# Kernel optimization log

Measured on AMD Instinct MI355X. Metric: run time of the kernel, lower is better.

Reference implementation:

```python
import jax, jax.numpy as jnp
import numpy as np

N_NODES = 30000
N_EDGES = 480000
IN_CH = 256
OUT_CH = 64
HEADS = 4
NEG_SLOPE = 0.2


def setup_inputs() -> dict:
    key = jax.random.key(0)
    ks = jax.random.split(key, 12)
    glorot = lambda k, shape: jax.random.normal(k, shape, jnp.float32) * (2.0 / (shape[0] + shape[-1])) ** 0.5
    x = jax.random.normal(ks[0], (N_NODES, IN_CH), jnp.float32)
    edge_index = jax.random.randint(ks[1], (2, N_EDGES), 0, N_NODES, dtype=jnp.int64)
    # gat1: in -> heads*out, concat=True
    W1 = glorot(ks[2], (IN_CH, HEADS * OUT_CH))
    att_src1 = glorot(ks[3], (HEADS, OUT_CH)) * 0.1
    att_dst1 = glorot(ks[4], (HEADS, OUT_CH)) * 0.1
    b1 = jnp.zeros((HEADS * OUT_CH,), jnp.float32)
    # gat2: heads*out -> out, 1 head
    W2 = glorot(ks[5], (HEADS * OUT_CH, OUT_CH))
    att_src2 = glorot(ks[6], (1, OUT_CH)) * 0.1
    att_dst2 = glorot(ks[7], (1, OUT_CH)) * 0.1
    b2 = jnp.zeros((OUT_CH,), jnp.float32)
    return {"x": x, "edge_index": edge_index, "W1": W1, "att_src1": att_src1,
            "att_dst1": att_dst1, "b1": b1, "W2": W2, "att_src2": att_src2,
            "att_dst2": att_dst2, "b2": b2}


def gat_conv(x, src, dst, W, att_src, att_dst, bias, heads, out_ch):
    """PyG GATConv (eval mode, add_self_loops already applied to src/dst).
    x: [N, F_in]; src/dst: [E] int; W: [F_in, heads*out_ch]; att_*: [heads, out_ch].
    Returns [N, heads*out_ch] (concatenated heads)."""
    N = x.shape[0]
    h = (x @ W).reshape(N, heads, out_ch)                     # [N,H,C]
    a_src = jnp.einsum('nhc,hc->nh', h, att_src)              # [N,H]
    a_dst = jnp.einsum('nhc,hc->nh', h, att_dst)              # [N,H]
    alpha = jax.nn.leaky_relu(a_src[src] + a_dst[dst], NEG_SLOPE)  # [E,H]
    # numerically stable softmax over edges grouped by destination node
    m = jax.ops.segment_max(alpha, dst, num_segments=N)       # [N,H]
    e = jnp.exp(alpha - m[dst])                               # [E,H]
    denom = jax.ops.segment_sum(e, dst, num_segments=N)       # [N,H]
    coef = e / denom[dst]                                     # [E,H]
    msg = h[src] * coef[:, :, None]                           # [E,H,C]
    out = jax.ops.segment_sum(msg, dst, num_segments=N)       # [N,H,C]
    return out.reshape(N, heads * out_ch) + bias


def reference(x, edge_index, W1, att_src1, att_dst1, b1, W2, att_src2, att_dst2, b2):
    N = x.shape[0]
    loops = jnp.arange(N, dtype=edge_index.dtype)
    src = jnp.concatenate([edge_index[0], loops])
    dst = jnp.concatenate([edge_index[1], loops])
    h = gat_conv(x, src, dst, W1, att_src1, att_dst1, b1, HEADS, OUT_CH)
    h = jax.nn.elu(h)
    out = gat_conv(h, src, dst, W2, att_src2, att_dst2, b2, 1, OUT_CH)
    return out
```

## Files before the change

kernel.cpp:

```cpp
#include <hip/hip_runtime.h>
#include <hip/hip_bf16.h>
#include <math.h>


#define NN 30000
#define NE 480000
#define CAP 64
#define GB1 469
#define FB1 469

typedef __attribute__((ext_vector_type(8))) short bf16x8;
typedef __attribute__((ext_vector_type(4))) float f32x4;

static constexpr size_t au(size_t x) { return (x + 255) & ~(size_t)255; }

static constexpr size_t SZ_H1B = (size_t)NN * 256 * 2;
static constexpr size_t SZ_HB  = (size_t)NN * 256 * 2;
static constexpr size_t SZ_H2B = (size_t)NN * 64 * 2;
static constexpr size_t SZ_W1T = 256 * 256 * 2;
static constexpr size_t SZ_W2T = 64 * 256 * 2;
static constexpr size_t SZ_AS1 = (size_t)NN * 4 * 4;
static constexpr size_t SZ_AS2 = (size_t)NN * 4;
static constexpr size_t SZ_CNT = (size_t)NN * 4;
static constexpr size_t SZ_CSR = (size_t)NN * CAP * 4;

static constexpr size_t OFF_H1B = 0;
static constexpr size_t OFF_HB  = OFF_H1B + au(SZ_H1B);
static constexpr size_t OFF_H2B = OFF_HB  + au(SZ_HB);
static constexpr size_t OFF_W1T = OFF_H2B + au(SZ_H2B);
static constexpr size_t OFF_W2T = OFF_W1T + au(SZ_W1T);
static constexpr size_t OFF_AS1 = OFF_W2T + au(SZ_W2T);
static constexpr size_t OFF_AD1 = OFF_AS1 + au(SZ_AS1);
static constexpr size_t OFF_AS2 = OFF_AD1 + au(SZ_AS1);
static constexpr size_t OFF_AD2 = OFF_AS2 + au(SZ_AS2);
static constexpr size_t OFF_CNT = OFF_AD2 + au(SZ_AS2);
static constexpr size_t OFF_CSR = OFF_CNT + au(SZ_CNT);

__device__ __forceinline__ float lrelu(float x) { return x > 0.f ? x : 0.2f * x; }
__device__ __forceinline__ float elu1(float x)  { return x > 0.f ? x : expm1f(x); }

__device__ __forceinline__ float bf2f(ushort u) {
    union { unsigned i; float f; } v; v.i = ((unsigned)u) << 16; return v.f;
}
__device__ __forceinline__ ushort f2bf(float f) {
    union { float f; unsigned i; } v; v.f = f;
    unsigned x = v.i;
    return (ushort)((x + 0x7FFFu + ((x >> 16) & 1u)) >> 16);
}


__global__ __launch_bounds__(256) void prep_kernel(const float* __restrict__ W1,
                                                   const float* __restrict__ W2,
                                                   ushort* __restrict__ w1t,
                                                   ushort* __restrict__ w2t,
                                                   int* __restrict__ cnt) {
    int i = blockIdx.x * 256 + threadIdx.x;
    if (i < NN) cnt[i] = 0;
    if (i < 256 * 256) {
        int r = i >> 8, c = i & 255;
        w1t[c * 256 + r] = f2bf(W1[i]);
    } else {
        int j = i - 256 * 256;
        if (j < 256 * 64) {
            int r = j >> 6, c = j & 63;
            w2t[c * 256 + r] = f2bf(W2[j]);
        }
    }
}


__global__ __launch_bounds__(256)
void g1f_kernel(const float* __restrict__ X, const ushort* __restrict__ BT,
                const float* __restrict__ att_s, const float* __restrict__ att_d,
                ushort* __restrict__ C, float* __restrict__ a_s,
                float* __restrict__ a_d, int M,
                const int* __restrict__ esrc, const int* __restrict__ edst,
                int* __restrict__ cnt, int* __restrict__ csr, int ne) {
    if (blockIdx.x & 1) {
        const int T = FB1 * 256;
        const int t = (blockIdx.x >> 1) * 256 + threadIdx.x;
        int s[4], d[4], pos[4];
        bool v[4];
#pragma unroll
        for (int j = 0; j < 4; ++j) {
            int i = t + j * T;
            v[j] = (i < ne);
            if (v[j]) { s[j] = esrc[i]; d[j] = edst[i]; }
        }
#pragma unroll
        for (int j = 0; j < 4; ++j)
            if (v[j]) pos[j] = atomicAdd(&cnt[d[j]], 1);
#pragma unroll
        for (int j = 0; j < 4; ++j)
            if (v[j] && pos[j] < CAP) csr[d[j] * CAP + pos[j]] = s[j];
        return;
    }
    constexpr int K = 256, N = 256;
    __shared__ float s_s[64 * 4], s_d[64 * 4];
    const int lane = threadIdx.x & 63;
    const int wn   = threadIdx.x >> 6;
    const int r  = lane & 15;
    const int kq = lane >> 4;
    const long rbase = (long)(blockIdx.x >> 1) * 64;
    const int  col0  = wn * 64;

    f32x4 acc[4][4] = {};
#pragma unroll 2
    for (int ks = 0; ks < K / 32; ++ks) {
        const int kb = ks * 32 + kq * 8;
        bf16x8 bfr[4];
#pragma unroll
        for (int n = 0; n < 4; ++n)
            bfr[n] = *(const bf16x8*)(BT + (long)(col0 + n * 16 + r) * K + kb);
#pragma unroll
        for (int m = 0; m < 4; ++m) {
            long rr = rbase + m * 16 + r; if (rr >= M) rr = M - 1;
            const float* xp = X + rr * (long)K + kb;
            f32x4 x0 = *(const f32x4*)xp;
            f32x4 x1 = *(const f32x4*)(xp + 4);
            bf16x8 afr;
            afr[0] = (short)f2bf(x0[0]); afr[1] = (short)f2bf(x0[1]);
            afr[2] = (short)f2bf(x0[2]); afr[3] = (short)f2bf(x0[3]);
            afr[4] = (short)f2bf(x1[0]); afr[5] = (short)f2bf(x1[1]);
            afr[6] = (short)f2bf(x1[2]); afr[7] = (short)f2bf(x1[3]);
#pragma unroll
            for (int n = 0; n < 4; ++n)
                acc[m][n] = __builtin_amdgcn_mfma_f32_16x16x32_bf16(afr, bfr[n], acc[m][n], 0, 0, 0);
        }
    }
#pragma unroll
    for (int m = 0; m < 4; ++m)
#pragma unroll
        for (int reg = 0; reg < 4; ++reg) {
            long rr = rbase + m * 16 + kq * 4 + reg;
            if (rr < M) {
                ushort* cp = C + rr * (long)N + col0 + r;
#pragma unroll
                for (int n = 0; n < 4; ++n) cp[n * 16] = f2bf(acc[m][n][reg]);
            }
        }
    float aws[4], awd[4];
#pragma unroll
    for (int n = 0; n < 4; ++n) {
        aws[n] = att_s[col0 + n * 16 + r];
        awd[n] = att_d[col0 + n * 16 + r];
    }
#pragma unroll
    for (int m = 0; m < 4; ++m)
#pragma unroll
        for (int reg = 0; reg < 4; ++reg) {
            float ps = acc[m][0][reg] * aws[0] + acc[m][1][reg] * aws[1]
                     + acc[m][2][reg] * aws[2] + acc[m][3][reg] * aws[3];
            float pd = acc[m][0][reg] * awd[0] + acc[m][1][reg] * awd[1]
                     + acc[m][2][reg] * awd[2] + acc[m][3][reg] * awd[3];
#pragma unroll
            for (int off = 1; off < 16; off <<= 1) {
                ps += __shfl_xor(ps, off, 64);
                pd += __shfl_xor(pd, off, 64);
            }
            if (r == 0) {
                int rl = m * 16 + kq * 4 + reg;
                s_s[rl * 4 + wn] = ps;
                s_d[rl * 4 + wn] = pd;
            }
        }
    __syncthreads();
    int t = threadIdx.x;
    long row = rbase + (t >> 2);
    if (row < M) {
        a_s[row * 4 + (t & 3)] = s_s[t];
        a_d[row * 4 + (t & 3)] = s_d[t];
    }
}


__global__ __launch_bounds__(256)
void gemm_att2_kernel(const ushort* __restrict__ A, const ushort* __restrict__ BT,
                      const float* __restrict__ att_s, const float* __restrict__ att_d,
                      ushort* __restrict__ C, float* __restrict__ a_s,
                      float* __restrict__ a_d, int M) {
    constexpr int K = 256, N = 64;
    const int lane = threadIdx.x & 63;
    const int wm   = threadIdx.x >> 6;
    const int r  = lane & 15;
    const int kq = lane >> 4;
    const long rbase = (long)blockIdx.x * 64 + wm * 16;

    f32x4 acc[4] = {};
#pragma unroll
    for (int ks = 0; ks < K / 32; ++ks) {
        const int kb = ks * 32 + kq * 8;
        long rr = rbase + r; if (rr >= M) rr = M - 1;
        bf16x8 afr = *(const bf16x8*)(A + rr * (long)K + kb);
#pragma unroll
        for (int n = 0; n < 4; ++n) {
            bf16x8 bfr = *(const bf16x8*)(BT + (long)(n * 16 + r) * K + kb);
            acc[n] = __builtin_amdgcn_mfma_f32_16x16x32_bf16(afr, bfr, acc[n], 0, 0, 0);
        }
    }
#pragma unroll
    for (int reg = 0; reg < 4; ++reg) {
        long rr = rbase + kq * 4 + reg;
        if (rr < M) {
            ushort* cp = C + rr * (long)N + r;
#pragma unroll
            for (int n = 0; n < 4; ++n) cp[n * 16] = f2bf(acc[n][reg]);
        }
    }
    float aws[4], awd[4];
#pragma unroll
    for (int n = 0; n < 4; ++n) {
        aws[n] = att_s[n * 16 + r];
        awd[n] = att_d[n * 16 + r];
    }
#pragma unroll
    for (int reg = 0; reg < 4; ++reg) {
        float ps = acc[0][reg] * aws[0] + acc[1][reg] * aws[1]
                 + acc[2][reg] * aws[2] + acc[3][reg] * aws[3];
        float pd = acc[0][reg] * awd[0] + acc[1][reg] * awd[1]
                 + acc[2][reg] * awd[2] + acc[3][reg] * awd[3];
#pragma unroll
        for (int off = 1; off < 16; off <<= 1) {
            ps += __shfl_xor(ps, off, 64);
            pd += __shfl_xor(pd, off, 64);
        }
        if (r == 0) {
            long row = rbase + kq * 4 + reg;
            if (row < M) { a_s[row] = ps; a_d[row] = pd; }
        }
    }
}


__global__ __launch_bounds__(256) void agg1_kernel(const ushort* __restrict__ h1b,
                                                   const float* __restrict__ a_s,
                                                   const float* __restrict__ a_d,
                                                   const int* __restrict__ cnt,
                                                   const int* __restrict__ csr,
                                                   const float* __restrict__ b1,
                                                   ushort* __restrict__ hb, int n_nodes) {
    const int lane = threadIdx.x & 63;
    const int n = blockIdx.x * 4 + (threadIdx.x >> 6);
    if (n >= n_nodes) return;
    const int head = lane >> 4;
    const float ad = a_d[(size_t)n * 4 + head];
    float acc0, acc1, acc2, acc3, ws;
    {
        float w = __expf(lrelu(a_s[(size_t)n * 4 + head] + ad));
        ushort4 hv = *(const ushort4*)(h1b + (size_t)n * 256 + 4 * lane);
        acc0 = w * bf2f(hv.x); acc1 = w * bf2f(hv.y);
        acc2 = w * bf2f(hv.z); acc3 = w * bf2f(hv.w);
        ws = w;
    }
    const int* bucket = csr + (size_t)n * CAP;
    const int deg = min(cnt[n], CAP);
    int e = 0;
    for (; e + 8 <= deg; e += 8) {
        int s[8];
#pragma unroll
        for (int j = 0; j < 8; ++j) s[j] = bucket[e + j];
        float q[8];
        ushort4 hv[8];
#pragma unroll
        for (int j = 0; j < 8; ++j) {
            q[j] = a_s[(size_t)s[j] * 4 + head];
            hv[j] = *(const ushort4*)(h1b + (size_t)s[j] * 256 + 4 * lane);
        }
#pragma unroll
        for (int j = 0; j < 8; ++j) {
            float w = __expf(lrelu(q[j] + ad));
            acc0 = fmaf(w, bf2f(hv[j].x), acc0);
            acc1 = fmaf(w, bf2f(hv[j].y), acc1);
            acc2 = fmaf(w, bf2f(hv[j].z), acc2);
            acc3 = fmaf(w, bf2f(hv[j].w), acc3);
            ws += w;
        }
    }
    for (; e + 4 <= deg; e += 4) {
        int s[4];
#pragma unroll
        for (int j = 0; j < 4; ++j) s[j] = bucket[e + j];
        float q[4];
        ushort4 hv[4];
#pragma unroll
        for (int j = 0; j < 4; ++j) {
            q[j] = a_s[(size_t)s[j] * 4 + head];
            hv[j] = *(const ushort4*)(h1b + (size_t)s[j] * 256 + 4 * lane);
        }
#pragma unroll
        for (int j = 0; j < 4; ++j) {
            float w = __expf(lrelu(q[j] + ad));
            acc0 = fmaf(w, bf2f(hv[j].x), acc0);
            acc1 = fmaf(w, bf2f(hv[j].y), acc1);
            acc2 = fmaf(w, bf2f(hv[j].z), acc2);
            acc3 = fmaf(w, bf2f(hv[j].w), acc3);
            ws += w;
        }
    }
    for (; e < deg; ++e) {
        int s = bucket[e];
        float w = __expf(lrelu(a_s[(size_t)s * 4 + head] + ad));
        ushort4 hv = *(const ushort4*)(h1b + (size_t)s * 256 + 4 * lane);
        acc0 = fmaf(w, bf2f(hv.x), acc0); acc1 = fmaf(w, bf2f(hv.y), acc1);
        acc2 = fmaf(w, bf2f(hv.z), acc2); acc3 = fmaf(w, bf2f(hv.w), acc3);
        ws += w;
    }
    float4 bv = *(const float4*)(b1 + 4 * lane);
    float inv = 1.f / ws;
    ushort4 o;
    o.x = f2bf(elu1(acc0 * inv + bv.x));
    o.y = f2bf(elu1(acc1 * inv + bv.y));
    o.z = f2bf(elu1(acc2 * inv + bv.z));
    o.w = f2bf(elu1(acc3 * inv + bv.w));
    *(ushort4*)(hb + (size_t)n * 256 + 4 * lane) = o;
}


__global__ __launch_bounds__(256) void agg2_kernel(const ushort* __restrict__ h2b,
                                                   const float* __restrict__ a_s,
                                                   const float* __restrict__ a_d,
                                                   const int* __restrict__ cnt,
                                                   const int* __restrict__ csr,
                                                   const float* __restrict__ b2,
                                                   float* __restrict__ out, int n_nodes) {
    const int lane = threadIdx.x & 63;
    const int n = blockIdx.x * 4 + (threadIdx.x >> 6);
    if (n >= n_nodes) return;
    const float ad = a_d[n];
    float w0 = __expf(lrelu(a_s[n] + ad));
    float acc = w0 * bf2f(h2b[(size_t)n * 64 + lane]);
    float ws = w0;
    const int* bucket = csr + (size_t)n * CAP;
    const int deg = min(cnt[n], CAP);
    int e = 0;
    for (; e + 8 <= deg; e += 8) {
        int s[8];
#pragma unroll
        for (int j = 0; j < 8; ++j) s[j] = bucket[e + j];
        float q[8];
        ushort hv[8];
#pragma unroll
        for (int j = 0; j < 8; ++j) {
            q[j] = a_s[s[j]];
            hv[j] = h2b[(size_t)s[j] * 64 + lane];
        }
#pragma unroll
        for (int j = 0; j < 8; ++j) {
            float w = __expf(lrelu(q[j] + ad));
            acc = fmaf(w, bf2f(hv[j]), acc);
            ws += w;
        }
    }
    for (; e < deg; ++e) {
        int s = bucket[e];
        float we = __expf(lrelu(a_s[s] + ad));
        acc = fmaf(we, bf2f(h2b[(size_t)s * 64 + lane]), acc);
        ws += we;
    }
    out[(size_t)n * 64 + lane] = acc / ws + b2[lane];
}


extern "C" void kernel_launch(void* const* d_in, const int* in_sizes, int n_in,
                              void* d_out, int out_size, void* d_ws, size_t ws_size,
                              hipStream_t stream) {
    const float* x      = (const float*)d_in[0];
    const int*   ei     = (const int*)d_in[1];
    const float* W1     = (const float*)d_in[2];
    const float* att_s1 = (const float*)d_in[3];
    const float* att_d1 = (const float*)d_in[4];
    const float* b1     = (const float*)d_in[5];
    const float* W2     = (const float*)d_in[6];
    const float* att_s2 = (const float*)d_in[7];
    const float* att_d2 = (const float*)d_in[8];
    const float* b2     = (const float*)d_in[9];
    float* out = (float*)d_out;

    char* ws = (char*)d_ws;
    ushort* h1b   = (ushort*)(ws + OFF_H1B);
    ushort* hb    = (ushort*)(ws + OFF_HB);
    ushort* h2b   = (ushort*)(ws + OFF_H2B);
    ushort* w1t   = (ushort*)(ws + OFF_W1T);
    ushort* w2t   = (ushort*)(ws + OFF_W2T);
    float* as1    = (float*)(ws + OFF_AS1);
    float* ad1    = (float*)(ws + OFF_AD1);
    float* as2    = (float*)(ws + OFF_AS2);
    float* ad2    = (float*)(ws + OFF_AD2);
    int* cnt      = (int*)(ws + OFF_CNT);
    int* csr      = (int*)(ws + OFF_CSR);

    const int* e_src = ei;
    const int* e_dst = ei + NE;

    const int gW = (NN + 3) / 4;

    prep_kernel<<<(256 * 256 + 256 * 64 + 255) / 256, 256, 0, stream>>>(W1, W2, w1t, w2t, cnt);

    g1f_kernel<<<2 * GB1, 256, 0, stream>>>(x, w1t, att_s1, att_d1,
                                            h1b, as1, ad1, NN,
                                            e_src, e_dst, cnt, csr, NE);

    agg1_kernel<<<gW, 256, 0, stream>>>(h1b, as1, ad1, cnt, csr, b1, hb, NN);

    gemm_att2_kernel<<<(NN + 63) / 64, 256, 0, stream>>>(hb, w2t, att_s2, att_d2,
                                                         h2b, as2, ad2, NN);
    agg2_kernel<<<gW, 256, 0, stream>>>(h2b, as2, ad2, cnt, csr, b2, out, NN);
}
```

Baseline: 138.9 us.

## Split fused GEMM/CSR-fill kernel back into separate fill and GEMM kernels

The earlier kernel interleaved CSR-fill blocks with layer-1 GEMM blocks in one launch so the atomic edge scatter could overlap the matmul. This change moves the fill into its own one-edge-per-thread kernel and runs the GEMM as a plain kernel afterwards. That removes the branch divergence and the odd/even block mapping, but it gives up the overlap and adds one more kernel launch.

```diff
diff --git a/kernel.cpp b/kernel.cpp
--- a/kernel.cpp
+++ b/kernel.cpp
@@ -6,8 +6,6 @@
 #define NN 30000
 #define NE 480000
 #define CAP 64
-#define GB1 469
-#define FB1 469
 
 typedef __attribute__((ext_vector_type(8))) short bf16x8;
 typedef __attribute__((ext_vector_type(4))) float f32x4;
@@ -69,39 +67,31 @@
 }
 
 
+__global__ __launch_bounds__(256) void fill_kernel(const int* __restrict__ src,
+                                                   const int* __restrict__ dst,
+                                                   int* __restrict__ cnt,
+                                                   int* __restrict__ csr, int e) {
+    int i = blockIdx.x * 256 + threadIdx.x;
+    if (i < e) {
+        int s = src[i], d = dst[i];
+        int pos = atomicAdd(&cnt[d], 1);
+        if (pos < CAP) csr[d * CAP + pos] = s;
+    }
+}
+
+
 __global__ __launch_bounds__(256)
-void g1f_kernel(const float* __restrict__ X, const ushort* __restrict__ BT,
-                const float* __restrict__ att_s, const float* __restrict__ att_d,
-                ushort* __restrict__ C, float* __restrict__ a_s,
-                float* __restrict__ a_d, int M,
-                const int* __restrict__ esrc, const int* __restrict__ edst,
-                int* __restrict__ cnt, int* __restrict__ csr, int ne) {
-    if (blockIdx.x & 1) {
-        const int T = FB1 * 256;
-        const int t = (blockIdx.x >> 1) * 256 + threadIdx.x;
-        int s[4], d[4], pos[4];
-        bool v[4];
-#pragma unroll
-        for (int j = 0; j < 4; ++j) {
-            int i = t + j * T;
-            v[j] = (i < ne);
-            if (v[j]) { s[j] = esrc[i]; d[j] = edst[i]; }
-        }
-#pragma unroll
-        for (int j = 0; j < 4; ++j)
-            if (v[j]) pos[j] = atomicAdd(&cnt[d[j]], 1);
-#pragma unroll
-        for (int j = 0; j < 4; ++j)
-            if (v[j] && pos[j] < CAP) csr[d[j] * CAP + pos[j]] = s[j];
-        return;
-    }
+void gemm_att1_kernel(const float* __restrict__ X, const ushort* __restrict__ BT,
+                      const float* __restrict__ att_s, const float* __restrict__ att_d,
+                      ushort* __restrict__ C, float* __restrict__ a_s,
+                      float* __restrict__ a_d, int M) {
     constexpr int K = 256, N = 256;
     __shared__ float s_s[64 * 4], s_d[64 * 4];
     const int lane = threadIdx.x & 63;
     const int wn   = threadIdx.x >> 6;
     const int r  = lane & 15;
     const int kq = lane >> 4;
-    const long rbase = (long)(blockIdx.x >> 1) * 64;
+    const long rbase = (long)blockIdx.x * 64;
     const int  col0  = wn * 64;
 
     f32x4 acc[4][4] = {};
@@ -392,14 +382,14 @@
     const int* e_src = ei;
     const int* e_dst = ei + NE;
 
+    const int gE = (NE + 255) / 256;
     const int gW = (NN + 3) / 4;
 
     prep_kernel<<<(256 * 256 + 256 * 64 + 255) / 256, 256, 0, stream>>>(W1, W2, w1t, w2t, cnt);
-
-    g1f_kernel<<<2 * GB1, 256, 0, stream>>>(x, w1t, att_s1, att_d1,
-                                            h1b, as1, ad1, NN,
-                                            e_src, e_dst, cnt, csr, NE);
-
+    fill_kernel<<<gE, 256, 0, stream>>>(e_src, e_dst, cnt, csr, NE);
+
+    gemm_att1_kernel<<<(NN + 63) / 64, 256, 0, stream>>>(x, w1t, att_s1, att_d1,
+                                                         h1b, as1, ad1, NN);
     agg1_kernel<<<gW, 256, 0, stream>>>(h1b, as1, ad1, cnt, csr, b1, hb, NN);
 
     gemm_att2_kernel<<<(NN + 63) / 64, 256, 0, stream>>>(hb, w2t, att_s2, att_d2,
```

New measurement: 137.0 us. About the same (-1.3%).
